# Optimization experiments

Measured on AMD Instinct MI355X. Metric: run time of the kernel, lower is better.

## Reference

```python
import jax, jax.numpy as jnp
import numpy as np


def _rope_tables(seq_len, d_k, dtype):
    # Faithful to SimpleRotary intent: only d_k//4 frequencies exist; the
    # remaining d_k//4 of the half-width table is identity (cos=1, sin=0),
    # i.e. zero angular frequency (modded-nanogpt style partial rotary).
    half = d_k // 2
    quarter = d_k // 4
    freqs = (1.0 / 10000.0) ** np.linspace(0.0, 1.0, quarter, dtype=np.float32)
    ang = np.concatenate([freqs, np.zeros(half - quarter, dtype=np.float32)])
    theta = np.arange(seq_len, dtype=np.float32)[:, None] * ang[None, :]  # [S, d_k//2]
    return jnp.asarray(np.cos(theta), dtype), jnp.asarray(np.sin(theta), dtype)


def _apply_rope(x, cos, sin):
    # x: [B, H, S, d_k]; cos/sin: [S, d_k//2]
    x1, x2 = jnp.split(x, 2, axis=-1)
    c = cos[None, None]  # [1,1,S,d_k//2]
    s = sin[None, None]
    return jnp.concatenate([x1 * c - x2 * s, x1 * s + x2 * c], axis=-1)


def setup_inputs() -> dict:
    key = jax.random.key(0)
    k1, k2, k3 = jax.random.split(key, 3)
    B, S, D = 2, 2048, 1024
    x = jax.random.normal(k1, (B, S, D), dtype=jnp.float32)
    Wqkv = jax.random.normal(k2, (3 * D, D), dtype=jnp.float32) * 0.02
    Wo = jax.random.normal(k3, (D, D), dtype=jnp.float32) * 0.02
    return {"x": x, "Wqkv": Wqkv, "Wo": Wo, "n_heads": 16}


def reference(x, Wqkv, Wo, n_heads):
    B, S, D = x.shape
    d_k = D // n_heads
    qkv = jnp.einsum('bsd,ed->bse', x, Wqkv)  # [B,S,3D]
    qkv = qkv.reshape(B, S, 3, n_heads, d_k).transpose(2, 0, 3, 1, 4)  # [3,B,H,S,d_k]
    q, k, v = qkv[0], qkv[1], qkv[2]
    cos, sin = _rope_tables(S, d_k, x.dtype)
    q = _apply_rope(q, cos, sin)
    k = _apply_rope(k, cos, sin)
    scale = 1.0 / float(np.sqrt(d_k))
    scores = jnp.einsum('bhqd,bhkd->bhqk', q, k) * scale  # [B,H,S,S]
    causal = jnp.tril(jnp.ones((S, S), dtype=bool))
    scores = jnp.where(causal[None, None], scores, jnp.finfo(scores.dtype).min)
    probs = jax.nn.softmax(scores, axis=-1)
    out = jnp.einsum('bhqk,bhkd->bhqd', probs, v)  # [B,H,S,d_k]
    out = out.transpose(0, 2, 1, 3).reshape(B, S, D)
    return jnp.einsum('bsd,ed->bse', out, Wo)
```

## Files before the change

### kernel.cpp

```cpp
#include <hip/hip_runtime.h>
#include <hip/hip_bf16.h>


typedef __bf16 bf16x8 __attribute__((ext_vector_type(8)));
typedef float f32x4 __attribute__((ext_vector_type(4)));

#define LOG2E 1.4426950408889634f

__device__ __forceinline__ ushort f2bf(float f) {
  __hip_bfloat16 h = __float2bfloat16(f);
  return __builtin_bit_cast(ushort, h);
}

__device__ __forceinline__ uint pack2(float a, float b) {
  return (uint)f2bf(a) | ((uint)f2bf(b) << 16);
}

__device__ __forceinline__ uint pack2t(float a, float b) {
  return __builtin_amdgcn_perm(__builtin_bit_cast(uint, b),
                               __builtin_bit_cast(uint, a), 0x07060302u);
}

__device__ __forceinline__ float fexp2(float x) {
#if __has_builtin(__builtin_amdgcn_exp2f)
  return __builtin_amdgcn_exp2f(x);
#else
  float r;
  asm volatile("v_exp_f32 %0, %1\n\ts_nop 0" : "=v"(r) : "v"(x));
  return r;
#endif
}

#define CBAR() __asm__ __volatile__("" ::: "memory")

__device__ __forceinline__ void gl2lds16(const ushort* g, ushort* l) {
  __builtin_amdgcn_global_load_lds(
      (const __attribute__((address_space(1))) void*)g,
      (__attribute__((address_space(3))) void*)l, 16, 0, 0);
}

__global__ __launch_bounds__(256) void conv_bf16(const float* __restrict__ src,
                                                 ushort* __restrict__ dst,
                                                 int n8) {
  int i = blockIdx.x * 256 + threadIdx.x;
  if (i >= n8) return;
  const float4* s = (const float4*)src + (long)i * 2;
  float4 a = s[0], b = s[1];
  uint4 pk = {pack2(a.x, a.y), pack2(a.z, a.w), pack2(b.x, b.y), pack2(b.z, b.w)};
  ((uint4*)dst)[i] = pk;
}

__global__ __launch_bounds__(256) void gemm_bt(
    const ushort* __restrict__ A, const ushort* __restrict__ B, int nbn,
    ushort* __restrict__ qb, ushort* __restrict__ kb, ushort* __restrict__ vb,
    float* __restrict__ Cout, int epi) {
  __shared__ __align__(16) ushort SMEM[17408];
  ushort* As = SMEM;
  ushort* Bs = SMEM + 8192;
  const int tid = threadIdx.x;
  const int w = tid >> 6, lane = tid & 63, quad = lane >> 4, lc = lane & 15;
  const int bid = blockIdx.x;
  const int bm = bid / nbn, bn = bid % nbn;
  const int wm = (w & 1) * 64, wn = (w >> 1) * 64;

  f32x4 acc[4][4] = {};

  const ushort* Ag = A + (long)bm * 131072;
  const ushort* Bg = B + (long)bn * 131072;

  for (int k0 = 0; k0 < 1024; k0 += 64) {
    __syncthreads();
    for (int i = 0; i < 4; ++i) {
      int u = i * 256 + tid;
      int row = u >> 3, ch = u & 7;
      gl2lds16(Ag + row * 1024 + k0 + ch * 8, &As[(i * 256 + w * 64) * 8]);
      gl2lds16(Bg + row * 1024 + k0 + ch * 8, &Bs[(i * 256 + w * 64) * 8]);
    }
    __builtin_amdgcn_s_waitcnt(0);
    __syncthreads();
    for (int kc = 0; kc < 2; ++kc) {
      bf16x8 af[4], bfr[4];
      for (int t = 0; t < 4; ++t)
        af[t] = *(const bf16x8*)&As[(wm + t * 16 + lc) * 64 + kc * 32 + quad * 8];
      for (int t = 0; t < 4; ++t)
        bfr[t] = *(const bf16x8*)&Bs[(wn + t * 16 + lc) * 64 + kc * 32 + quad * 8];
      for (int rt = 0; rt < 4; ++rt)
        for (int ct = 0; ct < 4; ++ct)
          acc[rt][ct] = __builtin_amdgcn_mfma_f32_16x16x32_bf16(
              af[rt], bfr[ct], acc[rt][ct], 0, 0, 0);
    }
  }

  if (epi == 0) {
    const int e0 = bn * 128;
    const int g = e0 >> 10;
    const int h0 = (e0 & 1023) >> 6;
    ushort* Ct = SMEM;
    __syncthreads();

    if (g == 2) {
      for (int rt = 0; rt < 4; ++rt)
        for (int ct = 0; ct < 4; ++ct) {
          int col = wn + ct * 16 + lc;
          int r0 = wm + rt * 16 + quad * 4;
          uint2 pk = {pack2(acc[rt][ct][0], acc[rt][ct][1]),
                      pack2(acc[rt][ct][2], acc[rt][ct][3])};
          *(uint2*)&Ct[col * 136 + r0] = pk;
        }
    } else {
      const float qs = (g == 0) ? 0.125f * LOG2E : 1.0f;
      const float ang = powf(1e-4f, (float)lc * (1.0f / 15.0f));
      for (int rt = 0; rt < 4; ++rt)
        for (int r = 0; r < 4; ++r) {
          int row = wm + rt * 16 + quad * 4 + r;
          int srow = (bm * 128 + row) & 2047;
          float theta = (float)srow * ang;
          float sn, c;
          sincosf(theta, &sn, &c);
          float x1 = acc[rt][0][r], x2 = acc[rt][2][r];
          acc[rt][0][r] = x1 * c - x2 * sn;
          acc[rt][2][r] = x1 * sn + x2 * c;
          for (int ct = 0; ct < 4; ++ct)
            Ct[row * 136 + wn + ct * 16 + lc] = f2bf(acc[rt][ct][r] * qs);
        }
    }
    __syncthreads();

    if (g == 0) {
      for (int i = 0; i < 8; ++i) {
        int u = i * 256 + tid;
        int row = u >> 4, c8 = u & 15;
        int m = bm * 128 + row;
        int srow = m & 2047, b = m >> 11;
        uint4 vv = *(const uint4*)&Ct[row * 136 + c8 * 8];
        *(uint4*)&qb[(((long)(b * 16 + h0 + (c8 >> 3))) * 2048 + srow) * 64 +
                     (c8 & 7) * 8] = vv;
      }
    } else if (g == 1) {
      for (int i = 0; i < 8; ++i) {
        int u = i * 256 + tid;
        int head = u >> 10, off = u & 1023;
        int jrel = off >> 9, kc = (off >> 8) & 1, t = (off >> 6) & 3;
        int quadK = (off >> 4) & 3, lcA = off & 15;
        int srl = jrel * 64 + t * 16 + lcA;
        uint4 vv = *(const uint4*)&Ct[srl * 136 + head * 64 + kc * 32 + quadK * 8];
        int m = bm * 128 + srl;
        int srow = m & 2047, b = m >> 11;
        int bh = b * 16 + h0 + head;
        int chunk = (srow >> 6) * 8 + kc * 4 + t;
        *(uint4*)&kb[(long)bh * 131072 + chunk * 512 + (quadK * 16 + lcA) * 8] = vv;
      }
    } else {
      for (int i = 0; i < 8; ++i) {
        int u = i * 256 + tid;
        int head = u >> 10, off = u & 1023;
        int jrel = off >> 9, kcV = (off >> 8) & 1, mt = (off >> 6) & 3;
        int quadV = (off >> 4) & 3, lcA = off & 15;
        int srl = jrel * 64 + kcV * 32 + quadV * 8;
        int d = mt * 16 + lcA;
        uint4 vv = *(const uint4*)&Ct[(head * 64 + d) * 136 + srl];
        int m = bm * 128 + srl;
        int srow = m & 2047, b = m >> 11;
        int bh = b * 16 + h0 + head;
        int chunk = (srow >> 6) * 8 + kcV * 4 + mt;
        *(uint4*)&vb[(long)bh * 131072 + chunk * 512 + (quadV * 16 + lcA) * 8] = vv;
      }
    }
  } else {
    const int row0 = bm * 128 + wm;
    for (int rt = 0; rt < 4; ++rt)
      for (int r = 0; r < 4; ++r) {
        int m = row0 + rt * 16 + quad * 4 + r;
        float* drow = Cout + (long)m * 1024 + bn * 128 + wn;
        for (int ct = 0; ct < 4; ++ct)
          drow[ct * 16 + lc] = acc[rt][ct][r];
      }
  }
}

__global__ __launch_bounds__(64) void attn_kernel(
    const ushort* __restrict__ qb, const ushort* __restrict__ kb,
    const ushort* __restrict__ vt, ushort* __restrict__ out) {
  __shared__ __align__(16) ushort Psw2[2][32 * 64];
  const int lane = threadIdx.x;
  const int quad = lane >> 4, lc = lane & 15, l7 = lc & 7;
  const int bid = blockIdx.x;
  const int s = 63 - (bid >> 5);
  const int bh = bid & 31;
  const int bidx = bh >> 4, h = bh & 15;
  const int qtbase = s * 32;

  bf16x8 qf[2][2];
  for (int kc = 0; kc < 2; ++kc)
    for (int q2 = 0; q2 < 2; ++q2)
      qf[kc][q2] = *(const bf16x8*)&qb[((long)bh * 2048 + qtbase + q2 * 16 + lc) * 64 +
                                       kc * 32 + quad * 8];

  f32x4 oacc[4][2] = {};
  float l_lane[2] = {0.0f, 0.0f};

  const ushort* K = kb + (long)bh * 131072;
  const ushort* Vt = vt + (long)bh * 131072;
  const int jmax = s >> 1;
  const int rowoff = (s & 1) * 32;
  const int lane8 = lane * 8;

#define LOADTILE(KF, VF, JT)                                                   \
  {                                                                            \
    const ushort* Kp_ = K + (JT) * 4096 + lane8;                               \
    const ushort* Vp_ = Vt + (JT) * 4096 + lane8;                              \
    for (int kc = 0; kc < 2; ++kc)                                             \
      for (int t = 0; t < 4; ++t) {                                            \
        KF[kc][t] = *(const bf16x8*)&Kp_[(kc * 4 + t) * 512];                  \
        VF[kc][t] = *(const bf16x8*)&Vp_[(kc * 4 + t) * 512];                  \
      }                                                                        \
  }

#define COMPUTE(KF, VF, J, PAR)                                                \
  {                                                                            \
    f32x4 sacc[4][2] = {};                                                     \
    for (int kc = 0; kc < 2; ++kc)                                             \
      for (int kt = 0; kt < 4; ++kt)                                           \
        for (int q2 = 0; q2 < 2; ++q2)                                         \
          sacc[kt][q2] = __builtin_amdgcn_mfma_f32_16x16x32_bf16(              \
              KF[kc][kt], qf[kc][q2], sacc[kt][q2], 0, 0, 0);                  \
    if ((J) == jmax) {                                \
      for (int kt = 0; kt < 4; ++kt)                                           \
        for (int q2 = 0; q2 < 2; ++q2) {                                       \
          int rowrel = rowoff + q2 * 16 + lc;                                  \
          for (int r = 0; r < 4; ++r)                                          \
            if (kt * 16 + quad * 4 + r > rowrel) sacc[kt][q2][r] = -1.0e30f;   \
        }                                                                      \
    }                                                                          \
    ushort* Psw = Psw2[PAR];                                                   \
    for (int q2 = 0; q2 < 2; ++q2) {                                           \
      float p[4][4];                                                           \
      float rs = 0.0f;                                                         \
      for (int kt = 0; kt < 4; ++kt)                                           \
        for (int r = 0; r < 4; ++r) {                                          \
          p[kt][r] = fexp2(sacc[kt][q2][r]);                                   \
          rs += p[kt][r];                                                      \
        }                                                                      \
      l_lane[q2] += rs;                                                        \
      for (int kt = 0; kt < 4; ++kt) {                                         \
        uint2 pk = {pack2t(p[kt][0], p[kt][1]), pack2t(p[kt][2], p[kt][3])};   \
        *(uint2*)&Psw[(q2 * 16 + lc) * 64 +                                    \
                      (((kt * 2 + (quad >> 1)) ^ l7) << 3) +                   \
                      ((quad & 1) << 2)] = pk;                                 \
      }                                                                        \
    }                                                                          \
    CBAR();       \
    for (int kc = 0; kc < 2; ++kc) {                                           \
      bf16x8 pf[2];                                                            \
      for (int q2 = 0; q2 < 2; ++q2)                                           \
        pf[q2] = *(const bf16x8*)&Psw[(q2 * 16 + lc) * 64 +                    \
                                      (((kc * 4 + quad) ^ l7) << 3)];          \
      for (int mt = 0; mt < 4; ++mt)                                           \
        for (int q2 = 0; q2 < 2; ++q2)                                         \
          oacc[mt][q2] = __builtin_amdgcn_mfma_f32_16x16x32_bf16(              \
              VF[kc][mt], pf[q2], oacc[mt][q2], 0, 0, 0);                      \
    }                                                                          \
  }

  bf16x8 kA[2][4], vA[2][4], kB[2][4], vB[2][4];
  LOADTILE(kA, vA, 0);
  int j = 0;
  while (true) {
    int jn = (j < jmax) ? j + 1 : j;
    LOADTILE(kB, vB, jn);
    COMPUTE(kA, vA, j, 0);
    if (j >= jmax) break;
    ++j;
    int jn2 = (j < jmax) ? j + 1 : j;
    LOADTILE(kA, vA, jn2);
    COMPUTE(kB, vB, j, 1);
    if (j >= jmax) break;
    ++j;
  }
#undef LOADTILE
#undef COMPUTE

  float l_[2];
  for (int q2 = 0; q2 < 2; ++q2) {
    float rs = l_lane[q2];
    rs += __shfl_xor(rs, 16, 64);
    rs += __shfl_xor(rs, 32, 64);
    l_[q2] = rs;
  }
  ushort* Psw = Psw2[0];
  CBAR();
  for (int q2 = 0; q2 < 2; ++q2) {
    float linv = 1.0f / l_[q2];
    for (int mt = 0; mt < 4; ++mt) {
      uint2 pk = {pack2(oacc[mt][q2][0] * linv, oacc[mt][q2][1] * linv),
                  pack2(oacc[mt][q2][2] * linv, oacc[mt][q2][3] * linv)};
      *(uint2*)&Psw[(q2 * 16 + lc) * 64 + (((mt * 2 + (quad >> 1)) ^ l7) << 3) +
                    ((quad & 1) << 2)] = pk;
    }
  }
  CBAR();
  {
    int r2 = lane >> 1;
    long mrow = (long)bidx * 2048 + qtbase + r2;
    for (int c = 0; c < 4; ++c) {
      int c8 = (lane & 1) * 4 + c;
      uint4 vv = *(const uint4*)&Psw[r2 * 64 + ((c8 ^ (r2 & 7)) << 3)];
      *(uint4*)&out[mrow * 1024 + h * 64 + c8 * 8] = vv;
    }
  }
}

extern "C" void kernel_launch(void* const* d_in, const int* in_sizes, int n_in,
                              void* d_out, int out_size, void* d_ws, size_t ws_size,
                              hipStream_t stream) {
  const float* x = nullptr;
  const float* Wqkv = nullptr;
  const float* Wo = nullptr;
  for (int i = 0; i < n_in; ++i) {
    if (in_sizes[i] == 4194304) x = (const float*)d_in[i];
    else if (in_sizes[i] == 3145728) Wqkv = (const float*)d_in[i];
    else if (in_sizes[i] == 1048576) Wo = (const float*)d_in[i];
  }
  float* out = (float*)d_out;

  ushort* qbuf = (ushort*)d_ws;
  ushort* kbuf = qbuf + 4194304;
  ushort* vbuf = kbuf + 4194304;
  ushort* scr4 = vbuf + 4194304;
  ushort* wqkvh = scr4;
  ushort* ao   = scr4;
  ushort* woh  = qbuf;
  ushort* xh   = (ushort*)d_out;

  conv_bf16<<<2048, 256, 0, stream>>>(x, xh, 524288);
  conv_bf16<<<1536, 256, 0, stream>>>(Wqkv, wqkvh, 393216);
  gemm_bt<<<768, 256, 0, stream>>>(xh, wqkvh, 24, qbuf, kbuf, vbuf, nullptr, 0);
  attn_kernel<<<2048, 64, 0, stream>>>(qbuf, kbuf, vbuf, ao);
  conv_bf16<<<512, 256, 0, stream>>>(Wo, woh, 131072);
  gemm_bt<<<256, 256, 0, stream>>>(ao, woh, 8, nullptr, nullptr, nullptr, out, 1);
}
```

Baseline: 196.6 us.

## Double-buffer GEMM K-loop with async LDS prefetch and merge conversion launches

The GEMM main loop now uses two LDS buffers with K-step 32, issuing global-to-LDS loads for the next tile before computing the current one and waiting with a partial vmcnt. This is meant to overlap memory latency with MFMA work instead of stalling on a full waitcnt each iteration. The LDS layout changes so each fragment is a contiguous lane*8 read, which should also avoid bank conflicts. Separately, the x and Wqkv fp32-to-bf16 conversions are merged into one launch to save launch overhead. The cost is twice as many barriers per K element and more reliance on exact vmcnt counting.

```diff
diff --git a/kernel.cpp b/kernel.cpp
--- a/kernel.cpp
+++ b/kernel.cpp
@@ -50,13 +50,30 @@
   ((uint4*)dst)[i] = pk;
 }
 
+__global__ __launch_bounds__(256) void conv_bf16_2(
+    const float* __restrict__ s0, ushort* __restrict__ d0, int n0,
+    const float* __restrict__ s1, ushort* __restrict__ d1, int n1) {
+  int i = blockIdx.x * 256 + threadIdx.x;
+  const float* src;
+  ushort* dst;
+  if (i < n0) {
+    src = s0; dst = d0;
+  } else {
+    i -= n0;
+    if (i >= n1) return;
+    src = s1; dst = d1;
+  }
+  const float4* s = (const float4*)src + (long)i * 2;
+  float4 a = s[0], b = s[1];
+  uint4 pk = {pack2(a.x, a.y), pack2(a.z, a.w), pack2(b.x, b.y), pack2(b.z, b.w)};
+  ((uint4*)dst)[i] = pk;
+}
+
 __global__ __launch_bounds__(256) void gemm_bt(
     const ushort* __restrict__ A, const ushort* __restrict__ B, int nbn,
     ushort* __restrict__ qb, ushort* __restrict__ kb, ushort* __restrict__ vb,
     float* __restrict__ Cout, int epi) {
   __shared__ __align__(16) ushort SMEM[17408];
-  ushort* As = SMEM;
-  ushort* Bs = SMEM + 8192;
   const int tid = threadIdx.x;
   const int w = tid >> 6, lane = tid & 63, quad = lane >> 4, lc = lane & 15;
   const int bid = blockIdx.x;
@@ -68,28 +85,51 @@
   const ushort* Ag = A + (long)bm * 131072;
   const ushort* Bg = B + (long)bn * 131072;
 
-  for (int k0 = 0; k0 < 1024; k0 += 64) {
-    __syncthreads();
-    for (int i = 0; i < 4; ++i) {
-      int u = i * 256 + tid;
-      int row = u >> 3, ch = u & 7;
-      gl2lds16(Ag + row * 1024 + k0 + ch * 8, &As[(i * 256 + w * 64) * 8]);
-      gl2lds16(Bg + row * 1024 + k0 + ch * 8, &Bs[(i * 256 + w * 64) * 8]);
-    }
-    __builtin_amdgcn_s_waitcnt(0);
-    __syncthreads();
-    for (int kc = 0; kc < 2; ++kc) {
+  const int rowc0 = w * 16 + (lane & 15);
+  const int colb = (lane >> 4) * 8;
+  const int aoff0 = rowc0 * 1024 + colb;
+  const int aoff1 = aoff0 + 65536;
+
+  ushort* b0 = SMEM;
+  ushort* b1 = SMEM + 8192;
+
+#define STAGE(BUF, K0)                                                         \
+  {                                                                            \
+    gl2lds16(Ag + aoff0 + (K0), (BUF) + w * 512);                              \
+    gl2lds16(Ag + aoff1 + (K0), (BUF) + (w + 4) * 512);                        \
+    gl2lds16(Bg + aoff0 + (K0), (BUF) + 4096 + w * 512);                       \
+    gl2lds16(Bg + aoff1 + (K0), (BUF) + 4096 + (w + 4) * 512);                 \
+  }
+
+  STAGE(b0, 0);
+  for (int k = 0; k < 32; ++k) {
+    ushort* cur = (k & 1) ? b1 : b0;
+    ushort* nxt = (k & 1) ? b0 : b1;
+    if (k < 31) {
+      STAGE(nxt, (k + 1) * 32);
+      asm volatile("s_waitcnt vmcnt(4)" ::: "memory");
+    } else {
+      asm volatile("s_waitcnt vmcnt(0)" ::: "memory");
+    }
+    CBAR();
+    __builtin_amdgcn_s_barrier();
+    CBAR();
+    {
+      const ushort* Ab = cur + (w & 1) * 2048 + lane * 8;
+      const ushort* Bb = cur + 4096 + (w >> 1) * 2048 + lane * 8;
       bf16x8 af[4], bfr[4];
-      for (int t = 0; t < 4; ++t)
-        af[t] = *(const bf16x8*)&As[(wm + t * 16 + lc) * 64 + kc * 32 + quad * 8];
-      for (int t = 0; t < 4; ++t)
-        bfr[t] = *(const bf16x8*)&Bs[(wn + t * 16 + lc) * 64 + kc * 32 + quad * 8];
+      for (int t = 0; t < 4; ++t) af[t] = *(const bf16x8*)&Ab[t * 512];
+      for (int t = 0; t < 4; ++t) bfr[t] = *(const bf16x8*)&Bb[t * 512];
       for (int rt = 0; rt < 4; ++rt)
         for (int ct = 0; ct < 4; ++ct)
           acc[rt][ct] = __builtin_amdgcn_mfma_f32_16x16x32_bf16(
               af[rt], bfr[ct], acc[rt][ct], 0, 0, 0);
     }
-  }
+    CBAR();
+    __builtin_amdgcn_s_barrier();
+    CBAR();
+  }
+#undef STAGE
 
   if (epi == 0) {
     const int e0 = bn * 128;
@@ -332,8 +372,7 @@
   ushort* woh  = qbuf;
   ushort* xh   = (ushort*)d_out;
 
-  conv_bf16<<<2048, 256, 0, stream>>>(x, xh, 524288);
-  conv_bf16<<<1536, 256, 0, stream>>>(Wqkv, wqkvh, 393216);
+  conv_bf16_2<<<3584, 256, 0, stream>>>(x, xh, 524288, Wqkv, wqkvh, 393216);
   gemm_bt<<<768, 256, 0, stream>>>(xh, wqkvh, 24, qbuf, kbuf, vbuf, nullptr, 0);
   attn_kernel<<<2048, 64, 0, stream>>>(qbuf, kbuf, vbuf, ao);
   conv_bf16<<<512, 256, 0, stream>>>(Wo, woh, 131072);
```

After: 203.4 us. 1.03x slower.
